# Optimization experiments

Measured on AMD Instinct MI355X. Metric: run time of the kernel, lower is better.

Reference implementation:

```python
import jax, jax.numpy as jnp
import numpy as np

N, K, D_IN, D_H, D_A, N_CLS = 8192, 10, 1024, 512, 256, 4


def setup_inputs() -> dict:
    key = jax.random.key(0)
    ks = jax.random.split(key, 20)
    def lin(k, fan_in, shape):
        return jax.random.normal(k, shape, dtype=jnp.float32) / np.sqrt(fan_in)
    return {
        "x_path": jax.random.normal(ks[0], (N, D_IN), dtype=jnp.float32),
        "cluster_id": jax.random.randint(ks[1], (N,), 0, K),
        # per-cluster phi MLP (Linear 1024->512, ReLU, Linear 512->512, ReLU); dropout = eval identity
        "W1": lin(ks[2], D_IN, (K, D_IN, D_H)), "b1": jnp.zeros((K, D_H), jnp.float32),
        "W2": lin(ks[3], D_H, (K, D_H, D_H)), "b2": jnp.zeros((K, D_H), jnp.float32),
        # attention_net fc: Linear 512->512 + ReLU
        "fc_W": lin(ks[4], D_H, (D_H, D_H)), "fc_b": jnp.zeros((D_H,), jnp.float32),
        # Attn_Net_Gated: a=tanh(Va), b=sigmoid(Vb), A=(a*b)@Vc
        "Va": lin(ks[5], D_H, (D_H, D_A)), "ba": jnp.zeros((D_A,), jnp.float32),
        "Vb": lin(ks[6], D_H, (D_H, D_A)), "bb": jnp.zeros((D_A,), jnp.float32),
        "Vc": lin(ks[7], D_A, (D_A, 1)), "bc": jnp.zeros((1,), jnp.float32),
        # rho: Linear 512->256 + ReLU
        "rho_W": lin(ks[8], D_H, (D_H, D_A)), "rho_b": jnp.zeros((D_A,), jnp.float32),
        # classifier: Linear 256->4
        "cls_W": lin(ks[9], D_A, (D_A, N_CLS)), "cls_b": jnp.zeros((N_CLS,), jnp.float32),
    }


def reference(x_path, cluster_id, W1, b1, W2, b2, fc_W, fc_b,
              Va, ba, Vb, bb, Vc, bc, rho_W, rho_b, cls_W, cls_b):
    # mask[k, n] = 1 if patch n belongs to cluster k
    mask = (cluster_id[None, :] == jnp.arange(K)[:, None]).astype(x_path.dtype)  # [K, N]

    # per-cluster 2-layer MLP applied to all patches, masked mean-pool (= AdaptiveAvgPool1d(1))
    def phi(W1i, b1i, W2i, b2i):
        h = jax.nn.relu(x_path @ W1i + b1i)          # [N, 512]
        return jax.nn.relu(h @ W2i + b2i)            # [N, 512]
    y = jax.vmap(phi)(W1, b1, W2, b2)                # [K, N, 512]
    cnt = mask.sum(axis=1)                           # [K]
    pooled = jnp.einsum('kn,knd->kd', mask, y) / jnp.maximum(cnt, 1.0)[:, None]  # [K, 512]
    # empty cluster -> zeros (matches torch.zeros((1,512)) branch since b terms are zero via where)
    pooled = jnp.where(cnt[:, None] > 0, pooled, 0.0)

    # attention_net: fc + gated attention
    h = jax.nn.relu(pooled @ fc_W + fc_b)            # [K, 512]
    a = jnp.tanh(h @ Va + ba)                        # [K, 256]
    b = jax.nn.sigmoid(h @ Vb + bb)                  # [K, 256]
    A = (a * b) @ Vc + bc                            # [K, 1]
    A = jax.nn.softmax(A.T, axis=1)                  # [1, K]
    h_path = A @ h                                   # [1, 512]
    h_path = jax.nn.relu(h_path @ rho_W + rho_b)[0]  # [256]
    logits = (h_path @ cls_W + cls_b)[None, :]       # [1, 4]
    Y_hat = jnp.argmax(logits, axis=1, keepdims=True)
    hazards = jax.nn.sigmoid(logits)
    S = jnp.cumprod(1.0 - hazards, axis=1)
    return hazards, S, Y_hat
```

## Files before the change

kernel.cpp:

```cpp
#include <hip/hip_runtime.h>
#include <math.h>

#define NPATCH 8192
#define KC     10
#define DIN    1024
#define DH     512
#define DA     256
#define NCLS   4

typedef unsigned short u16;
typedef short bf16x8 __attribute__((ext_vector_type(8)));
typedef float f32x4  __attribute__((ext_vector_type(4)));

#define OFF_CNT   0
#define OFF_BAR   48
#define OFF_IDX   64
#define OFF_PSUM  327744
#define OFF_H     348224
#define OFF_H2    368768
#define OFF_SRED  369792
#define OFF_W1P   373888
#define OFF_W2P   10859648
#define OFF_XC    16102528
#define OFF_H1    32879744

__device__ __forceinline__ u16 f2bf(float f) {
  union { float f; unsigned u; } v; v.f = f;
  unsigned r = (v.u + 0x7fffu + ((v.u >> 16) & 1u)) >> 16;
  return (u16)r;
}

struct __align__(8) U16x4 { u16 x, y, z, w; };

__device__ __forceinline__ void dma16(const u16* gp, u16* lp) {
  __builtin_amdgcn_global_load_lds(
      (const __attribute__((address_space(1))) void*)gp,
      (__attribute__((address_space(3))) void*)lp, 16, 0, 0);
}

#define W1_TILES (KC * (DIN / 32) * (DH / 32))
#define W2_TILES (KC * (DH / 32) * (DH / 32))
#define NB_BUCKET 32
#define NB_XCONV  256
#define WT_PER_BLK 4
#define NB_PREP (NB_BUCKET + NB_XCONV + (W1_TILES + W2_TILES) / WT_PER_BLK)

__global__ __launch_bounds__(256) void prep_kernel(
    const int* __restrict__ cid, int* __restrict__ cnt,
    int* __restrict__ idxlist, const float* __restrict__ W1,
    const float* __restrict__ W2, u16* __restrict__ W1p,
    u16* __restrict__ W2p, const float* __restrict__ x,
    u16* __restrict__ xc, float* __restrict__ psum) {
  int b = blockIdx.x, t = threadIdx.x;
  if (b < NB_BUCKET) {
    int g = b * 256 + t;
    if (g < KC * DH) psum[g] = 0.f;
    __shared__ int lcnt[KC], lbase[KC];
    if (t < KC) lcnt[t] = 0;
    __syncthreads();
    int n = b * 256 + t;
    int k = cid[n];
    int myoff = atomicAdd(&lcnt[k], 1);
    __syncthreads();
    if (t < KC) lbase[t] = atomicAdd(&cnt[t], lcnt[t]);
    __syncthreads();
    idxlist[k * NPATCH + lbase[k] + myoff] = n;
  } else if (b < NB_BUCKET + NB_XCONV) {
    int n = (b - NB_BUCKET) * 32 + (t >> 3);
    const float4* xp = (const float4*)(x + (size_t)n * DIN + (t & 7) * 128);
    U16x4* dst = (U16x4*)(xc + (size_t)n * DIN + (t & 7) * 128);
#pragma unroll
    for (int j = 0; j < 32; ++j) {
      float4 v = xp[j];
      U16x4 o = {f2bf(v.x), f2bf(v.y), f2bf(v.z), f2bf(v.w)};
      dst[j] = o;
    }
  } else {
    __shared__ u16 tile[32][33];
#pragma unroll
    for (int it = 0; it < WT_PER_BLK; ++it) {
      int bb = (b - NB_BUCKET - NB_XCONV) * WT_PER_BLK + it;
      const float* src;
      u16* dst;
      if (bb < W1_TILES) {
        int k = bb / 512, rem = bb % 512;
        int kb = rem / 16, n0 = (rem % 16) * 32;
        src = W1 + (size_t)k * DIN * DH + (size_t)kb * 32 * DH + n0;
        dst = W1p + (((size_t)(k * 32 + kb) * 512 + n0) * 32);
      } else {
        int b2 = bb - W1_TILES;
        int k = b2 / 256, rem = b2 % 256;
        int kb = rem / 16, n0 = (rem % 16) * 32;
        src = W2 + (size_t)k * DH * DH + (size_t)kb * 32 * DH + n0;
        dst = W2p + (((size_t)(k * 16 + kb) * 512 + n0) * 32);
      }
      {
        int ki = t >> 3, n4 = (t & 7) * 4;
        float4 v = *(const float4*)&src[(size_t)ki * DH + n4];
        tile[ki][n4 + 0] = f2bf(v.x);
        tile[ki][n4 + 1] = f2bf(v.y);
        tile[ki][n4 + 2] = f2bf(v.z);
        tile[ki][n4 + 3] = f2bf(v.w);
      }
      __syncthreads();
      {
        int n = t >> 3, ki = (t & 7) * 4;
        U16x4 o = {tile[ki + 0][n], tile[ki + 1][n], tile[ki + 2][n],
                   tile[ki + 3][n]};
        int kis = ki ^ (((n >> 1) & 3) << 3);
        *(U16x4*)&dst[(size_t)n * 32 + kis] = o;
      }
      __syncthreads();
    }
  }
}


__global__ __launch_bounds__(512, 2) void phi1_kernel(
    const u16* __restrict__ xc, const u16* __restrict__ W1p,
    const float* __restrict__ b1, const int* __restrict__ cnt,
    const int* __restrict__ idxlist, u16* __restrict__ h1) {
  const int slice = blockIdx.x, k = blockIdx.y, chunk = blockIdx.z;
  const int cntk = cnt[k];
  const int base = chunk * 256;
  if (base >= cntk) return;

  const int tid = threadIdx.x;
  const int w = tid >> 6, lane = tid & 63;
  const int quad = lane >> 4, l16 = lane & 15;
  const int wr = w >> 1, wc = w & 1;
  const int rl = lane >> 2, gl = lane & 3;
  const int gsw = gl ^ ((rl >> 1) & 3);
  const int rsw = (quad ^ ((l16 >> 1) & 3)) << 3;

  __shared__ __align__(16) u16 lds[24576];
  u16* As = lds;
  u16* Bs = lds + 16384;

  int ridx[2];
#pragma unroll
  for (int jj = 0; jj < 2; ++jj) {
    int row_l = (w * 2 + jj) * 16 + rl;
    ridx[jj] = (base + row_l < cntk) ? idxlist[k * NPATCH + base + row_l] : 0;
  }
  const u16* bsrc =
      W1p + ((size_t)(k * 32) * 512 + slice * 128 + w * 16 + rl) * 32 + gl * 8;

#pragma unroll
  for (int jj = 0; jj < 2; ++jj)
    dma16(xc + (size_t)ridx[jj] * DIN + gsw * 8,
          As + (w * 2 + jj) * 512);
  dma16(bsrc, Bs + w * 512);

  const f32x4 zero4 = {0.f, 0.f, 0.f, 0.f};
  f32x4 acc[4][4];
#pragma unroll
  for (int fr = 0; fr < 4; ++fr)
#pragma unroll
    for (int fc = 0; fc < 4; ++fc) acc[fr][fc] = zero4;

  for (int t = 0; t < 32; ++t) {
    const int buf = t & 1;
    if (t < 31) {
      const int bn = buf ^ 1, tn = t + 1;
#pragma unroll
      for (int jj = 0; jj < 2; ++jj)
        dma16(xc + (size_t)ridx[jj] * DIN + tn * 32 + gsw * 8,
              As + bn * 8192 + (w * 2 + jj) * 512);
      dma16(bsrc + (size_t)tn * 16384, Bs + bn * 4096 + w * 512);
      asm volatile("s_waitcnt vmcnt(3)" ::: "memory");
    } else {
      asm volatile("s_waitcnt vmcnt(0)" ::: "memory");
    }
    __syncthreads();
    bf16x8 af[4], bfr[4];
#pragma unroll
    for (int fr = 0; fr < 4; ++fr) {
      int row = wr * 64 + fr * 16 + l16;
      af[fr] = *(const bf16x8*)&As[buf * 8192 + row * 32 + rsw];
    }
#pragma unroll
    for (int fc = 0; fc < 4; ++fc) {
      int col = wc * 64 + fc * 16 + l16;
      bfr[fc] = *(const bf16x8*)&Bs[buf * 4096 + col * 32 + rsw];
    }
#pragma unroll
    for (int fr = 0; fr < 4; ++fr)
#pragma unroll
      for (int fc = 0; fc < 4; ++fc)
        acc[fr][fc] = __builtin_amdgcn_mfma_f32_16x16x32_bf16(
            af[fr], bfr[fc], acc[fr][fc], 0, 0, 0);
    __syncthreads();
  }

#pragma unroll
  for (int half = 0; half < 2; ++half) {
    __syncthreads();
    if ((wr >> 1) == half) {
#pragma unroll
      for (int fr = 0; fr < 4; ++fr)
#pragma unroll
        for (int fc = 0; fc < 4; ++fc) {
          int col = wc * 64 + fc * 16 + l16;
          float bias = b1[k * DH + slice * 128 + col];
#pragma unroll
          for (int r = 0; r < 4; ++r) {
            int lrow = (wr & 1) * 64 + fr * 16 + quad * 4 + r;
            lds[lrow * 136 + col] = f2bf(fmaxf(acc[fr][fc][r] + bias, 0.f));
          }
        }
    }
    __syncthreads();
    {
      int lrow = tid >> 2, seg = tid & 3;
      int brow = base + half * 128 + lrow;
      if (brow < cntk) {
        int n = idxlist[k * NPATCH + brow];
        u16* dst = h1 + (size_t)n * DH + slice * 128 + seg * 32;
#pragma unroll
        for (int j = 0; j < 4; ++j)
          *(bf16x8*)(dst + j * 8) =
              *(const bf16x8*)&lds[lrow * 136 + seg * 32 + j * 8];
      }
    }
  }
}

__global__ __launch_bounds__(512, 2) void phi2_kernel(
    const u16* __restrict__ h1, const u16* __restrict__ W2p,
    const float* __restrict__ b2, const int* __restrict__ cnt,
    const int* __restrict__ idxlist, float* __restrict__ psum) {
  const int slice = blockIdx.x, k = blockIdx.y, chunk = blockIdx.z;
  const int cntk = cnt[k];
  const int base = chunk * 256;
  if (base >= cntk) return;

  const int tid = threadIdx.x;
  const int w = tid >> 6, lane = tid & 63;
  const int quad = lane >> 4, l16 = lane & 15;
  const int wr = w >> 1, wc = w & 1;
  const int rl = lane >> 2, gl = lane & 3;
  const int gsw = gl ^ ((rl >> 1) & 3);
  const int rsw = (quad ^ ((l16 >> 1) & 3)) << 3;

  __shared__ __align__(16) u16 lds[24576];
  u16* As = lds;
  u16* Bs = lds + 16384;

  int ridx[2];
#pragma unroll
  for (int jj = 0; jj < 2; ++jj) {
    int row_l = (w * 2 + jj) * 16 + rl;
    ridx[jj] = (base + row_l < cntk) ? idxlist[k * NPATCH + base + row_l] : 0;
  }
  const u16* bsrc =
      W2p + ((size_t)(k * 16) * 512 + slice * 128 + w * 16 + rl) * 32 + gl * 8;

#pragma unroll
  for (int jj = 0; jj < 2; ++jj)
    dma16(h1 + (size_t)ridx[jj] * DH + gsw * 8, As + (w * 2 + jj) * 512);
  dma16(bsrc, Bs + w * 512);

  const f32x4 zero4 = {0.f, 0.f, 0.f, 0.f};
  f32x4 acc[4][4];
#pragma unroll
  for (int fr = 0; fr < 4; ++fr)
#pragma unroll
    for (int fc = 0; fc < 4; ++fc) acc[fr][fc] = zero4;

  for (int t = 0; t < 16; ++t) {
    const int buf = t & 1;
    if (t < 15) {
      const int bn = buf ^ 1, tn = t + 1;
#pragma unroll
      for (int jj = 0; jj < 2; ++jj)
        dma16(h1 + (size_t)ridx[jj] * DH + tn * 32 + gsw * 8,
              As + bn * 8192 + (w * 2 + jj) * 512);
      dma16(bsrc + (size_t)tn * 16384, Bs + bn * 4096 + w * 512);
      asm volatile("s_waitcnt vmcnt(3)" ::: "memory");
    } else {
      asm volatile("s_waitcnt vmcnt(0)" ::: "memory");
    }
    __syncthreads();
    bf16x8 af[4], bfr[4];
#pragma unroll
    for (int fr = 0; fr < 4; ++fr) {
      int row = wr * 64 + fr * 16 + l16;
      af[fr] = *(const bf16x8*)&As[buf * 8192 + row * 32 + rsw];
    }
#pragma unroll
    for (int fc = 0; fc < 4; ++fc) {
      int col = wc * 64 + fc * 16 + l16;
      bfr[fc] = *(const bf16x8*)&Bs[buf * 4096 + col * 32 + rsw];
    }
#pragma unroll
    for (int fr = 0; fr < 4; ++fr)
#pragma unroll
      for (int fc = 0; fc < 4; ++fc)
        acc[fr][fc] = __builtin_amdgcn_mfma_f32_16x16x32_bf16(
            af[fr], bfr[fc], acc[fr][fc], 0, 0, 0);
    __syncthreads();
  }

#pragma unroll
  for (int fc = 0; fc < 4; ++fc) {
    int col = wc * 64 + fc * 16 + l16;
    float bias = b2[k * DH + slice * 128 + col];
    float sv = 0.f;
#pragma unroll
    for (int fr = 0; fr < 4; ++fr)
#pragma unroll
      for (int r = 0; r < 4; ++r) {
        int row = base + wr * 64 + fr * 16 + quad * 4 + r;
        sv += (row < cntk) ? fmaxf(acc[fr][fc][r] + bias, 0.f) : 0.f;
      }
    sv += __shfl_xor(sv, 16, 64);
    sv += __shfl_xor(sv, 32, 64);
    if (quad == 0) atomicAdd(&psum[k * DH + slice * 128 + col], sv);
  }
}

#define NTB 64

__device__ __forceinline__ void bar_arrive_wait(int* bar) {
  __syncthreads();
  if (threadIdx.x == 0) {
    __threadfence();
    __hip_atomic_fetch_add(bar, 1, __ATOMIC_RELEASE, __HIP_MEMORY_SCOPE_AGENT);
    while (__hip_atomic_load(bar, __ATOMIC_ACQUIRE,
                             __HIP_MEMORY_SCOPE_AGENT) < NTB) {
      __builtin_amdgcn_s_sleep(1);
    }
  }
  __syncthreads();
}

__global__ __launch_bounds__(256) void tail_kernel(
    const float* __restrict__ psum, const int* __restrict__ cnt,
    const float* __restrict__ fcW, const float* __restrict__ fcb,
    const float* __restrict__ Va, const float* __restrict__ ba,
    const float* __restrict__ Vb, const float* __restrict__ bb_,
    const float* __restrict__ Vc, const float* __restrict__ rhoW,
    const float* __restrict__ rhob, const float* __restrict__ clsW,
    const float* __restrict__ clsb, float* __restrict__ hstore,
    float* __restrict__ sred, float* __restrict__ h2g,
    int* __restrict__ bar, float* __restrict__ out) {
  __shared__ float p_sh[KC * DH];
  __shared__ float r1[2560];
  __shared__ float r2[2560];
  __shared__ float invs[KC];
  __shared__ float gate_sh[4 * KC];
  __shared__ float ws_sh[KC];
  __shared__ float hp_sh[DH];
  const int tid = threadIdx.x;
  const int b = blockIdx.x;

  if (tid < KC) {
    int c = cnt[tid];
    invs[tid] = (c > 0) ? 1.f / (float)c : 0.f;
  }
  __syncthreads();
#pragma unroll
  for (int it = 0; it < KC * DH / 256; ++it) {
    int e = it * 256 + tid;
    p_sh[e] = psum[e] * invs[e >> 9];
  }
  __syncthreads();
  {
    const int jj = tid & 7, dq = tid >> 3;
    const int j0 = b * 8;
    float acc[KC];
#pragma unroll
    for (int k = 0; k < KC; ++k) acc[k] = 0.f;
#pragma unroll 4
    for (int i = 0; i < 16; ++i) {
      int d = dq * 16 + i;
      float wv = fcW[(size_t)d * DH + j0 + jj];
#pragma unroll
      for (int k = 0; k < KC; ++k) acc[k] = fmaf(p_sh[k * DH + d], wv, acc[k]);
    }
#pragma unroll
    for (int k = 0; k < KC; ++k) r1[(dq * 8 + jj) * KC + k] = acc[k];
    __syncthreads();
    if (tid < 8 * KC) {
      int jj2 = tid / KC, k = tid % KC;
      float s = 0.f;
#pragma unroll
      for (int q = 0; q < 32; ++q) s += r1[(q * 8 + jj2) * KC + k];
      hstore[k * DH + j0 + jj2] = fmaxf(s + fcb[j0 + jj2], 0.f);
    }
  }
  bar_arrive_wait(&bar[0]);

#pragma unroll
  for (int it = 0; it < KC * DH / 256; ++it) {
    int e = it * 256 + tid;
    p_sh[e] = hstore[e];
  }
  __syncthreads();
  {
    const int jj = tid & 3, dq = tid >> 2;
    const int j0 = b * 4;
    float sa[KC], sb[KC];
#pragma unroll
    for (int k = 0; k < KC; ++k) { sa[k] = 0.f; sb[k] = 0.f; }
#pragma unroll 4
    for (int i = 0; i < 8; ++i) {
      int d = dq * 8 + i;
      float va = Va[(size_t)d * DA + j0 + jj];
      float vb = Vb[(size_t)d * DA + j0 + jj];
#pragma unroll
      for (int k = 0; k < KC; ++k) {
        float h = p_sh[k * DH + d];
        sa[k] = fmaf(h, va, sa[k]);
        sb[k] = fmaf(h, vb, sb[k]);
      }
    }
#pragma unroll
    for (int k = 0; k < KC; ++k) {
      r1[(dq * 4 + jj) * KC + k] = sa[k];
      r2[(dq * 4 + jj) * KC + k] = sb[k];
    }
    __syncthreads();
    if (tid < 4 * KC) {
      int jj2 = tid / KC, k = tid % KC;
      float ta = 0.f, tb = 0.f;
#pragma unroll
      for (int q = 0; q < 64; ++q) {
        ta += r1[(q * 4 + jj2) * KC + k];
        tb += r2[(q * 4 + jj2) * KC + k];
      }
      float a = tanhf(ta + ba[j0 + jj2]);
      float g = 1.f / (1.f + expf(-(tb + bb_[j0 + jj2])));
      gate_sh[jj2 * KC + k] = a * g * Vc[j0 + jj2];
    }
    __syncthreads();
    if (tid < KC) {
      float s = 0.f;
#pragma unroll
      for (int jj2 = 0; jj2 < 4; ++jj2) s += gate_sh[jj2 * KC + tid];
      sred[b * 16 + tid] = s;
    }
  }
  bar_arrive_wait(&bar[1]);

  if (tid < KC) {
    float s = 0.f;
    for (int q = 0; q < NTB; ++q) s += sred[q * 16 + tid];
    ws_sh[tid] = s;
  }
  __syncthreads();
  if (tid == 0) {
    float m = -1e30f;
#pragma unroll
    for (int k2 = 0; k2 < KC; ++k2) m = fmaxf(m, ws_sh[k2]);
    float Z = 0.f;
#pragma unroll
    for (int k2 = 0; k2 < KC; ++k2) {
      float e = expf(ws_sh[k2] - m);
      ws_sh[k2] = e;
      Z += e;
    }
    float iZ = 1.f / Z;
#pragma unroll
    for (int k2 = 0; k2 < KC; ++k2) ws_sh[k2] *= iZ;
  }
  __syncthreads();
#pragma unroll
  for (int it = 0; it < 2; ++it) {
    int d = it * 256 + tid;
    float s = 0.f;
#pragma unroll
    for (int k2 = 0; k2 < KC; ++k2) s = fmaf(ws_sh[k2], p_sh[k2 * DH + d], s);
    hp_sh[d] = s;
  }
  __syncthreads();
  {
    const int jj = tid & 3, dq = tid >> 2;
    const int j0 = b * 4;
    float acc = 0.f;
#pragma unroll 4
    for (int i = 0; i < 8; ++i) {
      int d = dq * 8 + i;
      acc = fmaf(hp_sh[d], rhoW[(size_t)d * DA + j0 + jj], acc);
    }
    r1[dq * 4 + jj] = acc;
    __syncthreads();
    if (tid < 4) {
      float s = 0.f;
#pragma unroll
      for (int q = 0; q < 64; ++q) s += r1[q * 4 + tid];
      h2g[j0 + tid] = fmaxf(s + rhob[j0 + tid], 0.f);
    }
  }

  if (b != 0) {
    __syncthreads();
    if (tid == 0) {
      __threadfence();
      __hip_atomic_fetch_add(&bar[2], 1, __ATOMIC_RELEASE,
                             __HIP_MEMORY_SCOPE_AGENT);
    }
    return;
  }
  bar_arrive_wait(&bar[2]);
  {
    float h = h2g[tid];
#pragma unroll
    for (int c = 0; c < NCLS; ++c)
      r1[c * 256 + tid] = h * clsW[(size_t)tid * NCLS + c];
    __syncthreads();
    for (int s = 128; s > 0; s >>= 1) {
      if (tid < s) {
#pragma unroll
        for (int c = 0; c < NCLS; ++c)
          r1[c * 256 + tid] += r1[c * 256 + tid + s];
      }
      __syncthreads();
    }
    if (tid == 0) {
      float lg[NCLS], hz[NCLS];
      int best = 0;
#pragma unroll
      for (int c = 0; c < NCLS; ++c) {
        lg[c] = r1[c * 256] + clsb[c];
        hz[c] = 1.f / (1.f + expf(-lg[c]));
        if (lg[c] > lg[best]) best = c;
      }
      float S = 1.f;
#pragma unroll
      for (int c = 0; c < NCLS; ++c) out[c] = hz[c];
#pragma unroll
      for (int c = 0; c < NCLS; ++c) {
        S *= (1.f - hz[c]);
        out[NCLS + c] = S;
      }
      out[2 * NCLS] = (float)best;
    }
  }
}

extern "C" void kernel_launch(void* const* d_in, const int* in_sizes, int n_in,
                              void* d_out, int out_size, void* d_ws,
                              size_t ws_size, hipStream_t stream) {
  const float* x    = (const float*)d_in[0];
  const int*   cid  = (const int*)d_in[1];
  const float* W1   = (const float*)d_in[2];
  const float* b1   = (const float*)d_in[3];
  const float* W2   = (const float*)d_in[4];
  const float* b2   = (const float*)d_in[5];
  const float* fcW  = (const float*)d_in[6];
  const float* fcb  = (const float*)d_in[7];
  const float* Va   = (const float*)d_in[8];
  const float* ba   = (const float*)d_in[9];
  const float* Vb   = (const float*)d_in[10];
  const float* bb_  = (const float*)d_in[11];
  const float* Vc   = (const float*)d_in[12];
  const float* rhoW = (const float*)d_in[14];
  const float* rhob = (const float*)d_in[15];
  const float* clsW = (const float*)d_in[16];
  const float* clsb = (const float*)d_in[17];
  float* out = (float*)d_out;

  char* ws = (char*)d_ws;
  int*   cnt     = (int*)(ws + OFF_CNT);
  int*   bar     = (int*)(ws + OFF_BAR);
  int*   idxlist = (int*)(ws + OFF_IDX);
  float* psum    = (float*)(ws + OFF_PSUM);
  float* hstore  = (float*)(ws + OFF_H);
  float* h2g     = (float*)(ws + OFF_H2);
  float* sred    = (float*)(ws + OFF_SRED);
  u16*   W1p     = (u16*)(ws + OFF_W1P);
  u16*   W2p     = (u16*)(ws + OFF_W2P);
  u16*   xc      = (u16*)(ws + OFF_XC);
  u16*   h1      = (u16*)(ws + OFF_H1);

  (void)hipMemsetAsync(cnt, 0, 64, stream);
  prep_kernel<<<NB_PREP, 256, 0, stream>>>(cid, cnt, idxlist, W1, W2, W1p, W2p,
                                           x, xc, psum);
  phi1_kernel<<<dim3(4, KC, 32), 512, 0, stream>>>(xc, W1p, b1, cnt, idxlist,
                                                   h1);
  phi2_kernel<<<dim3(4, KC, 32), 512, 0, stream>>>(h1, W2p, b2, cnt, idxlist,
                                                   psum);
  tail_kernel<<<NTB, 256, 0, stream>>>(psum, cnt, fcW, fcb, Va, ba, Vb, bb_,
                                       Vc, rhoW, rhob, clsW, clsb, hstore,
                                       sred, h2g, bar, out);
}
```

Baseline: 220.5 us.

## Fuse prep and both phi GEMMs into one persistent kernel with grid barriers

Merges the bucketing/weight-conversion prep, phi1 and phi2 into a single persistent 256-block kernel separated by software grid barriers. x rows are gathered into cluster-sorted contiguous order during bf16 conversion, so the GEMMs read contiguous rows instead of indirect idxlist gathers, and h1 is written contiguously. Tiles shrink to 128 rows and work units are packed across clusters, which avoids the empty chunks launched by the old fixed 32-chunk grid. The cost is the grid-barrier spin overhead, a reliance on all 256 blocks being co-resident, and lower per-block reuse from the smaller tiles.

```diff
diff --git a/kernel.cpp b/kernel.cpp
--- a/kernel.cpp
+++ b/kernel.cpp
@@ -14,9 +14,9 @@
 
 #define OFF_CNT   0
 #define OFF_BAR   48
-#define OFF_IDX   64
-#define OFF_PSUM  327744
-#define OFF_H     348224
+#define OFF_IDX   128
+#define OFF_PSUM  327808
+#define OFF_H     348288
 #define OFF_H2    368768
 #define OFF_SRED  369792
 #define OFF_W1P   373888
@@ -40,46 +40,61 @@
 
 #define W1_TILES (KC * (DIN / 32) * (DH / 32))
 #define W2_TILES (KC * (DH / 32) * (DH / 32))
-#define NB_BUCKET 32
-#define NB_XCONV  256
-#define WT_PER_BLK 4
-#define NB_PREP (NB_BUCKET + NB_XCONV + (W1_TILES + W2_TILES) / WT_PER_BLK)
-
-__global__ __launch_bounds__(256) void prep_kernel(
+#define NMB 256
+
+__device__ __forceinline__ void gbar(int* bar, int target) {
+  __syncthreads();
+  if (threadIdx.x == 0) {
+    __threadfence();
+    __hip_atomic_fetch_add(bar, 1, __ATOMIC_RELEASE, __HIP_MEMORY_SCOPE_AGENT);
+    while (__hip_atomic_load(bar, __ATOMIC_ACQUIRE,
+                             __HIP_MEMORY_SCOPE_AGENT) < target) {
+      __builtin_amdgcn_s_sleep(1);
+    }
+  }
+  __syncthreads();
+}
+
+__global__ __launch_bounds__(512, 2) void mega_kernel(
     const int* __restrict__ cid, int* __restrict__ cnt,
     int* __restrict__ idxlist, const float* __restrict__ W1,
     const float* __restrict__ W2, u16* __restrict__ W1p,
     u16* __restrict__ W2p, const float* __restrict__ x,
-    u16* __restrict__ xc, float* __restrict__ psum) {
-  int b = blockIdx.x, t = threadIdx.x;
-  if (b < NB_BUCKET) {
-    int g = b * 256 + t;
-    if (g < KC * DH) psum[g] = 0.f;
-    __shared__ int lcnt[KC], lbase[KC];
-    if (t < KC) lcnt[t] = 0;
-    __syncthreads();
-    int n = b * 256 + t;
-    int k = cid[n];
-    int myoff = atomicAdd(&lcnt[k], 1);
-    __syncthreads();
-    if (t < KC) lbase[t] = atomicAdd(&cnt[t], lcnt[t]);
-    __syncthreads();
-    idxlist[k * NPATCH + lbase[k] + myoff] = n;
-  } else if (b < NB_BUCKET + NB_XCONV) {
-    int n = (b - NB_BUCKET) * 32 + (t >> 3);
-    const float4* xp = (const float4*)(x + (size_t)n * DIN + (t & 7) * 128);
-    U16x4* dst = (U16x4*)(xc + (size_t)n * DIN + (t & 7) * 128);
-#pragma unroll
-    for (int j = 0; j < 32; ++j) {
-      float4 v = xp[j];
-      U16x4 o = {f2bf(v.x), f2bf(v.y), f2bf(v.z), f2bf(v.w)};
-      dst[j] = o;
-    }
-  } else {
-    __shared__ u16 tile[32][33];
-#pragma unroll
-    for (int it = 0; it < WT_PER_BLK; ++it) {
-      int bb = (b - NB_BUCKET - NB_XCONV) * WT_PER_BLK + it;
+    u16* __restrict__ xc, const float* __restrict__ b1,
+    const float* __restrict__ b2, u16* __restrict__ h1,
+    float* __restrict__ psum, int* __restrict__ bar) {
+  __shared__ __align__(16) u16 lds[17408];
+  __shared__ u16 wtile[2][32][33];
+  __shared__ int lcnt[KC], lbase[KC];
+
+  const int b = blockIdx.x, tid = threadIdx.x;
+  const int w = tid >> 6, lane = tid & 63;
+  const int quad = lane >> 4, l16 = lane & 15;
+  const int wr = w & 3, wc = w >> 2;
+  const int rl = lane >> 2, gl = lane & 3;
+  const int gsw = gl ^ ((rl >> 1) & 3);
+  const int rsw = (quad ^ ((l16 >> 1) & 3)) << 3;
+
+  if (b < 32) {
+    if (tid < KC) lcnt[tid] = 0;
+    __syncthreads();
+    int myk = 0, myoff = 0;
+    if (tid < 256) {
+      myk = cid[b * 256 + tid];
+      myoff = atomicAdd(&lcnt[myk], 1);
+    }
+    __syncthreads();
+    if (tid < KC) lbase[tid] = atomicAdd(&cnt[tid], lcnt[tid]);
+    __syncthreads();
+    if (tid < 256) idxlist[myk * NPATCH + lbase[myk] + myoff] = b * 256 + tid;
+  }
+  if (b == 32) {
+    for (int e = tid; e < KC * DH; e += 512) psum[e] = 0.f;
+  }
+  {
+    const int sub = tid >> 8, tt = tid & 255;
+    for (int i = 0; i < 15; ++i) {
+      int bb = i * 512 + b * 2 + sub;
       const float* src;
       u16* dst;
       if (bb < W1_TILES) {
@@ -88,235 +103,239 @@
         src = W1 + (size_t)k * DIN * DH + (size_t)kb * 32 * DH + n0;
         dst = W1p + (((size_t)(k * 32 + kb) * 512 + n0) * 32);
       } else {
-        int b2 = bb - W1_TILES;
-        int k = b2 / 256, rem = b2 % 256;
+        int b2_ = bb - W1_TILES;
+        int k = b2_ / 256, rem = b2_ % 256;
         int kb = rem / 16, n0 = (rem % 16) * 32;
         src = W2 + (size_t)k * DH * DH + (size_t)kb * 32 * DH + n0;
         dst = W2p + (((size_t)(k * 16 + kb) * 512 + n0) * 32);
       }
       {
-        int ki = t >> 3, n4 = (t & 7) * 4;
+        int ki = tt >> 3, n4 = (tt & 7) * 4;
         float4 v = *(const float4*)&src[(size_t)ki * DH + n4];
-        tile[ki][n4 + 0] = f2bf(v.x);
-        tile[ki][n4 + 1] = f2bf(v.y);
-        tile[ki][n4 + 2] = f2bf(v.z);
-        tile[ki][n4 + 3] = f2bf(v.w);
+        wtile[sub][ki][n4 + 0] = f2bf(v.x);
+        wtile[sub][ki][n4 + 1] = f2bf(v.y);
+        wtile[sub][ki][n4 + 2] = f2bf(v.z);
+        wtile[sub][ki][n4 + 3] = f2bf(v.w);
       }
       __syncthreads();
       {
-        int n = t >> 3, ki = (t & 7) * 4;
-        U16x4 o = {tile[ki + 0][n], tile[ki + 1][n], tile[ki + 2][n],
-                   tile[ki + 3][n]};
+        int n = tt >> 3, ki = (tt & 7) * 4;
+        U16x4 o = {wtile[sub][ki + 0][n], wtile[sub][ki + 1][n],
+                   wtile[sub][ki + 2][n], wtile[sub][ki + 3][n]};
         int kis = ki ^ (((n >> 1) & 3) << 3);
         *(U16x4*)&dst[(size_t)n * 32 + kis] = o;
       }
       __syncthreads();
     }
   }
-}
-
-
-__global__ __launch_bounds__(512, 2) void phi1_kernel(
-    const u16* __restrict__ xc, const u16* __restrict__ W1p,
-    const float* __restrict__ b1, const int* __restrict__ cnt,
-    const int* __restrict__ idxlist, u16* __restrict__ h1) {
-  const int slice = blockIdx.x, k = blockIdx.y, chunk = blockIdx.z;
-  const int cntk = cnt[k];
-  const int base = chunk * 256;
-  if (base >= cntk) return;
-
-  const int tid = threadIdx.x;
-  const int w = tid >> 6, lane = tid & 63;
-  const int quad = lane >> 4, l16 = lane & 15;
-  const int wr = w >> 1, wc = w & 1;
-  const int rl = lane >> 2, gl = lane & 3;
-  const int gsw = gl ^ ((rl >> 1) & 3);
-  const int rsw = (quad ^ ((l16 >> 1) & 3)) << 3;
-
-  __shared__ __align__(16) u16 lds[24576];
+  gbar(&bar[0], NMB);
+
+  int cn[KC];
+#pragma unroll
+  for (int i = 0; i < KC; ++i) cn[i] = cnt[i];
+
+  {
+    int rowc = b * 32 + (tid >> 4);
+    int kk = 0, accp = 0;
+#pragma unroll
+    for (int i = 0; i < KC - 1; ++i) {
+      accp += cn[i];
+      if (rowc >= accp) kk = i + 1;
+    }
+    int cbase = 0;
+#pragma unroll
+    for (int i = 0; i < KC - 1; ++i) cbase += (i < kk) ? cn[i] : 0;
+    int src = idxlist[kk * NPATCH + rowc - cbase];
+    const float4* xp = (const float4*)(x + (size_t)src * DIN + (tid & 15) * 64);
+    U16x4* dst = (U16x4*)(xc + (size_t)rowc * DIN + (tid & 15) * 64);
+#pragma unroll
+    for (int j = 0; j < 16; ++j) {
+      float4 v = xp[j];
+      U16x4 o = {f2bf(v.x), f2bf(v.y), f2bf(v.z), f2bf(v.w)};
+      dst[j] = o;
+    }
+  }
+  gbar(&bar[1], NMB);
+
+  int nch[KC], NU = 0;
+#pragma unroll
+  for (int i = 0; i < KC; ++i) {
+    nch[i] = (cn[i] + 127) >> 7;
+    NU += nch[i];
+  }
+
   u16* As = lds;
-  u16* Bs = lds + 16384;
-
-  int ridx[2];
-#pragma unroll
-  for (int jj = 0; jj < 2; ++jj) {
-    int row_l = (w * 2 + jj) * 16 + rl;
-    ridx[jj] = (base + row_l < cntk) ? idxlist[k * NPATCH + base + row_l] : 0;
-  }
-  const u16* bsrc =
-      W1p + ((size_t)(k * 32) * 512 + slice * 128 + w * 16 + rl) * 32 + gl * 8;
-
-#pragma unroll
-  for (int jj = 0; jj < 2; ++jj)
-    dma16(xc + (size_t)ridx[jj] * DIN + gsw * 8,
-          As + (w * 2 + jj) * 512);
-  dma16(bsrc, Bs + w * 512);
+  u16* Bs = lds + 8192;
 
   const f32x4 zero4 = {0.f, 0.f, 0.f, 0.f};
-  f32x4 acc[4][4];
-#pragma unroll
-  for (int fr = 0; fr < 4; ++fr)
-#pragma unroll
-    for (int fc = 0; fc < 4; ++fc) acc[fr][fc] = zero4;
-
-  for (int t = 0; t < 32; ++t) {
-    const int buf = t & 1;
-    if (t < 31) {
-      const int bn = buf ^ 1, tn = t + 1;
-#pragma unroll
-      for (int jj = 0; jj < 2; ++jj)
-        dma16(xc + (size_t)ridx[jj] * DIN + tn * 32 + gsw * 8,
-              As + bn * 8192 + (w * 2 + jj) * 512);
-      dma16(bsrc + (size_t)tn * 16384, Bs + bn * 4096 + w * 512);
-      asm volatile("s_waitcnt vmcnt(3)" ::: "memory");
-    } else {
-      asm volatile("s_waitcnt vmcnt(0)" ::: "memory");
-    }
-    __syncthreads();
-    bf16x8 af[4], bfr[4];
-#pragma unroll
-    for (int fr = 0; fr < 4; ++fr) {
-      int row = wr * 64 + fr * 16 + l16;
-      af[fr] = *(const bf16x8*)&As[buf * 8192 + row * 32 + rsw];
-    }
+
+  for (int u = b; u < 4 * NU; u += NMB) {
+    const int slice = u & 3;
+    int c = u >> 2, kk = 0;
+#pragma unroll
+    for (int i = 0; i < KC - 1; ++i) {
+      if (c >= nch[i]) { c -= nch[i]; kk = i + 1; }
+    }
+    int cbase = 0;
+#pragma unroll
+    for (int i = 0; i < KC - 1; ++i) cbase += (i < kk) ? cn[i] : 0;
+    const int cntk = cn[kk];
+    const int base = c * 128;
+
+    __syncthreads();
+
+    int grow = cbase + base + w * 16 + rl;
+    if (grow > NPATCH - 1) grow = NPATCH - 1;
+    const u16* asrc = xc + (size_t)grow * DIN + gsw * 8;
+    const u16* bsrc =
+        W1p + ((size_t)(kk * 32) * 512 + slice * 128 + w * 16 + rl) * 32 +
+        gl * 8;
+
+    dma16(asrc, As + w * 512);
+    dma16(bsrc, Bs + w * 512);
+
+    f32x4 acc[2][4];
+#pragma unroll
+    for (int fr = 0; fr < 2; ++fr)
+#pragma unroll
+      for (int fc = 0; fc < 4; ++fc) acc[fr][fc] = zero4;
+
+    for (int t = 0; t < 32; ++t) {
+      const int buf = t & 1;
+      if (t < 31) {
+        const int bn = buf ^ 1;
+        dma16(asrc + (t + 1) * 32, As + bn * 4096 + w * 512);
+        dma16(bsrc + (size_t)(t + 1) * 16384, Bs + bn * 4096 + w * 512);
+        asm volatile("s_waitcnt vmcnt(2)" ::: "memory");
+      } else {
+        asm volatile("s_waitcnt vmcnt(0)" ::: "memory");
+      }
+      __syncthreads();
+      bf16x8 af[2], bfr[4];
+#pragma unroll
+      for (int fr = 0; fr < 2; ++fr) {
+        int row = wr * 32 + fr * 16 + l16;
+        af[fr] = *(const bf16x8*)&As[buf * 4096 + row * 32 + rsw];
+      }
+#pragma unroll
+      for (int fc = 0; fc < 4; ++fc) {
+        int col = wc * 64 + fc * 16 + l16;
+        bfr[fc] = *(const bf16x8*)&Bs[buf * 4096 + col * 32 + rsw];
+      }
+#pragma unroll
+      for (int fr = 0; fr < 2; ++fr)
+#pragma unroll
+        for (int fc = 0; fc < 4; ++fc)
+          acc[fr][fc] = __builtin_amdgcn_mfma_f32_16x16x32_bf16(
+              af[fr], bfr[fc], acc[fr][fc], 0, 0, 0);
+      __syncthreads();
+    }
+
+#pragma unroll
+    for (int fr = 0; fr < 2; ++fr)
+#pragma unroll
+      for (int fc = 0; fc < 4; ++fc) {
+        int col = wc * 64 + fc * 16 + l16;
+        float bias = b1[kk * DH + slice * 128 + col];
+#pragma unroll
+        for (int r = 0; r < 4; ++r) {
+          int row = wr * 32 + fr * 16 + quad * 4 + r;
+          lds[row * 136 + col] = f2bf(fmaxf(acc[fr][fc][r] + bias, 0.f));
+        }
+      }
+    __syncthreads();
+    {
+      int row = tid >> 2, seg = tid & 3;
+      if (base + row < cntk) {
+        u16* dst = h1 + (size_t)(cbase + base + row) * DH + slice * 128 +
+                   seg * 32;
+#pragma unroll
+        for (int j = 0; j < 4; ++j)
+          *(bf16x8*)(dst + j * 8) =
+              *(const bf16x8*)&lds[row * 136 + seg * 32 + j * 8];
+      }
+    }
+  }
+  gbar(&bar[2], NMB);
+
+  for (int u = b; u < 4 * NU; u += NMB) {
+    const int slice = u & 3;
+    int c = u >> 2, kk = 0;
+#pragma unroll
+    for (int i = 0; i < KC - 1; ++i) {
+      if (c >= nch[i]) { c -= nch[i]; kk = i + 1; }
+    }
+    int cbase = 0;
+#pragma unroll
+    for (int i = 0; i < KC - 1; ++i) cbase += (i < kk) ? cn[i] : 0;
+    const int cntk = cn[kk];
+    const int base = c * 128;
+
+    __syncthreads();
+
+    int grow = cbase + base + w * 16 + rl;
+    if (grow > NPATCH - 1) grow = NPATCH - 1;
+    const u16* asrc = h1 + (size_t)grow * DH + gsw * 8;
+    const u16* bsrc =
+        W2p + ((size_t)(kk * 16) * 512 + slice * 128 + w * 16 + rl) * 32 +
+        gl * 8;
+
+    dma16(asrc, As + w * 512);
+    dma16(bsrc, Bs + w * 512);
+
+    f32x4 acc[2][4];
+#pragma unroll
+    for (int fr = 0; fr < 2; ++fr)
+#pragma unroll
+      for (int fc = 0; fc < 4; ++fc) acc[fr][fc] = zero4;
+
+    for (int t = 0; t < 16; ++t) {
+      const int buf = t & 1;
+      if (t < 15) {
+        const int bn = buf ^ 1;
+        dma16(asrc + (t + 1) * 32, As + bn * 4096 + w * 512);
+        dma16(bsrc + (size_t)(t + 1) * 16384, Bs + bn * 4096 + w * 512);
+        asm volatile("s_waitcnt vmcnt(2)" ::: "memory");
+      } else {
+        asm volatile("s_waitcnt vmcnt(0)" ::: "memory");
+      }
+      __syncthreads();
+      bf16x8 af[2], bfr[4];
+#pragma unroll
+      for (int fr = 0; fr < 2; ++fr) {
+        int row = wr * 32 + fr * 16 + l16;
+        af[fr] = *(const bf16x8*)&As[buf * 4096 + row * 32 + rsw];
+      }
+#pragma unroll
+      for (int fc = 0; fc < 4; ++fc) {
+        int col = wc * 64 + fc * 16 + l16;
+        bfr[fc] = *(const bf16x8*)&Bs[buf * 4096 + col * 32 + rsw];
+      }
+#pragma unroll
+      for (int fr = 0; fr < 2; ++fr)
+#pragma unroll
+        for (int fc = 0; fc < 4; ++fc)
+          acc[fr][fc] = __builtin_amdgcn_mfma_f32_16x16x32_bf16(
+              af[fr], bfr[fc], acc[fr][fc], 0, 0, 0);
+      __syncthreads();
+    }
+
 #pragma unroll
     for (int fc = 0; fc < 4; ++fc) {
       int col = wc * 64 + fc * 16 + l16;
-      bfr[fc] = *(const bf16x8*)&Bs[buf * 4096 + col * 32 + rsw];
-    }
-#pragma unroll
-    for (int fr = 0; fr < 4; ++fr)
-#pragma unroll
-      for (int fc = 0; fc < 4; ++fc)
-        acc[fr][fc] = __builtin_amdgcn_mfma_f32_16x16x32_bf16(
-            af[fr], bfr[fc], acc[fr][fc], 0, 0, 0);
-    __syncthreads();
-  }
-
-#pragma unroll
-  for (int half = 0; half < 2; ++half) {
-    __syncthreads();
-    if ((wr >> 1) == half) {
-#pragma unroll
-      for (int fr = 0; fr < 4; ++fr)
-#pragma unroll
-        for (int fc = 0; fc < 4; ++fc) {
-          int col = wc * 64 + fc * 16 + l16;
-          float bias = b1[k * DH + slice * 128 + col];
-#pragma unroll
-          for (int r = 0; r < 4; ++r) {
-            int lrow = (wr & 1) * 64 + fr * 16 + quad * 4 + r;
-            lds[lrow * 136 + col] = f2bf(fmaxf(acc[fr][fc][r] + bias, 0.f));
-          }
+      float bias = b2[kk * DH + slice * 128 + col];
+      float sv = 0.f;
+#pragma unroll
+      for (int fr = 0; fr < 2; ++fr)
+#pragma unroll
+        for (int r = 0; r < 4; ++r) {
+          int row = base + wr * 32 + fr * 16 + quad * 4 + r;
+          sv += (row < cntk) ? fmaxf(acc[fr][fc][r] + bias, 0.f) : 0.f;
         }
-    }
-    __syncthreads();
-    {
-      int lrow = tid >> 2, seg = tid & 3;
-      int brow = base + half * 128 + lrow;
-      if (brow < cntk) {
-        int n = idxlist[k * NPATCH + brow];
-        u16* dst = h1 + (size_t)n * DH + slice * 128 + seg * 32;
-#pragma unroll
-        for (int j = 0; j < 4; ++j)
-          *(bf16x8*)(dst + j * 8) =
-              *(const bf16x8*)&lds[lrow * 136 + seg * 32 + j * 8];
-      }
-    }
-  }
-}
-
-__global__ __launch_bounds__(512, 2) void phi2_kernel(
-    const u16* __restrict__ h1, const u16* __restrict__ W2p,
-    const float* __restrict__ b2, const int* __restrict__ cnt,
-    const int* __restrict__ idxlist, float* __restrict__ psum) {
-  const int slice = blockIdx.x, k = blockIdx.y, chunk = blockIdx.z;
-  const int cntk = cnt[k];
-  const int base = chunk * 256;
-  if (base >= cntk) return;
-
-  const int tid = threadIdx.x;
-  const int w = tid >> 6, lane = tid & 63;
-  const int quad = lane >> 4, l16 = lane & 15;
-  const int wr = w >> 1, wc = w & 1;
-  const int rl = lane >> 2, gl = lane & 3;
-  const int gsw = gl ^ ((rl >> 1) & 3);
-  const int rsw = (quad ^ ((l16 >> 1) & 3)) << 3;
-
-  __shared__ __align__(16) u16 lds[24576];
-  u16* As = lds;
-  u16* Bs = lds + 16384;
-
-  int ridx[2];
-#pragma unroll
-  for (int jj = 0; jj < 2; ++jj) {
-    int row_l = (w * 2 + jj) * 16 + rl;
-    ridx[jj] = (base + row_l < cntk) ? idxlist[k * NPATCH + base + row_l] : 0;
-  }
-  const u16* bsrc =
-      W2p + ((size_t)(k * 16) * 512 + slice * 128 + w * 16 + rl) * 32 + gl * 8;
-
-#pragma unroll
-  for (int jj = 0; jj < 2; ++jj)
-    dma16(h1 + (size_t)ridx[jj] * DH + gsw * 8, As + (w * 2 + jj) * 512);
-  dma16(bsrc, Bs + w * 512);
-
-  const f32x4 zero4 = {0.f, 0.f, 0.f, 0.f};
-  f32x4 acc[4][4];
-#pragma unroll
-  for (int fr = 0; fr < 4; ++fr)
-#pragma unroll
-    for (int fc = 0; fc < 4; ++fc) acc[fr][fc] = zero4;
-
-  for (int t = 0; t < 16; ++t) {
-    const int buf = t & 1;
-    if (t < 15) {
-      const int bn = buf ^ 1, tn = t + 1;
-#pragma unroll
-      for (int jj = 0; jj < 2; ++jj)
-        dma16(h1 + (size_t)ridx[jj] * DH + tn * 32 + gsw * 8,
-              As + bn * 8192 + (w * 2 + jj) * 512);
-      dma16(bsrc + (size_t)tn * 16384, Bs + bn * 4096 + w * 512);
-      asm volatile("s_waitcnt vmcnt(3)" ::: "memory");
-    } else {
-      asm volatile("s_waitcnt vmcnt(0)" ::: "memory");
-    }
-    __syncthreads();
-    bf16x8 af[4], bfr[4];
-#pragma unroll
-    for (int fr = 0; fr < 4; ++fr) {
-      int row = wr * 64 + fr * 16 + l16;
-      af[fr] = *(const bf16x8*)&As[buf * 8192 + row * 32 + rsw];
-    }
-#pragma unroll
-    for (int fc = 0; fc < 4; ++fc) {
-      int col = wc * 64 + fc * 16 + l16;
-      bfr[fc] = *(const bf16x8*)&Bs[buf * 4096 + col * 32 + rsw];
-    }
-#pragma unroll
-    for (int fr = 0; fr < 4; ++fr)
-#pragma unroll
-      for (int fc = 0; fc < 4; ++fc)
-        acc[fr][fc] = __builtin_amdgcn_mfma_f32_16x16x32_bf16(
-            af[fr], bfr[fc], acc[fr][fc], 0, 0, 0);
-    __syncthreads();
-  }
-
-#pragma unroll
-  for (int fc = 0; fc < 4; ++fc) {
-    int col = wc * 64 + fc * 16 + l16;
-    float bias = b2[k * DH + slice * 128 + col];
-    float sv = 0.f;
-#pragma unroll
-    for (int fr = 0; fr < 4; ++fr)
-#pragma unroll
-      for (int r = 0; r < 4; ++r) {
-        int row = base + wr * 64 + fr * 16 + quad * 4 + r;
-        sv += (row < cntk) ? fmaxf(acc[fr][fc][r] + bias, 0.f) : 0.f;
-      }
-    sv += __shfl_xor(sv, 16, 64);
-    sv += __shfl_xor(sv, 32, 64);
-    if (quad == 0) atomicAdd(&psum[k * DH + slice * 128 + col], sv);
+      sv += __shfl_xor(sv, 16, 64);
+      sv += __shfl_xor(sv, 32, 64);
+      if (quad == 0) atomicAdd(&psum[kk * DH + slice * 128 + col], sv);
+    }
   }
 }
 
@@ -575,14 +594,10 @@
   u16*   xc      = (u16*)(ws + OFF_XC);
   u16*   h1      = (u16*)(ws + OFF_H1);
 
-  (void)hipMemsetAsync(cnt, 0, 64, stream);
-  prep_kernel<<<NB_PREP, 256, 0, stream>>>(cid, cnt, idxlist, W1, W2, W1p, W2p,
-                                           x, xc, psum);
-  phi1_kernel<<<dim3(4, KC, 32), 512, 0, stream>>>(xc, W1p, b1, cnt, idxlist,
-                                                   h1);
-  phi2_kernel<<<dim3(4, KC, 32), 512, 0, stream>>>(h1, W2p, b2, cnt, idxlist,
-                                                   psum);
+  (void)hipMemsetAsync(cnt, 0, 128, stream);
+  mega_kernel<<<NMB, 512, 0, stream>>>(cid, cnt, idxlist, W1, W2, W1p, W2p, x,
+                                       xc, b1, b2, h1, psum, bar);
   tail_kernel<<<NTB, 256, 0, stream>>>(psum, cnt, fcW, fcb, Va, ba, Vb, bb_,
                                        Vc, rhoW, rhob, clsW, clsb, hstore,
-                                       sred, h2g, bar, out);
+                                       sred, h2g, bar + 3, out);
 }
```

Result: slower. 420.4 us (+90.7%).
